# Kernel optimization log

Hardware: AMD Instinct MI355X
Metric: run time of the kernel (lower is better)

Reference implementation:

```python
import jax, jax.numpy as jnp
import numpy as np

N_BITS = 8
QMAX = float(2 ** (N_BITS - 1) - 1)  # 127 for 8-bit symmetric
EPS = 1e-8


def fake_quant(x, axes):
    """Symmetric fake quantization (quantize + dequantize) over `axes`.

    scale = amax(|x|) / qmax over the reduction axes, then
    round/clamp to the integer grid and rescale back to float.
    """
    amax = jnp.max(jnp.abs(x), axis=axes, keepdims=True)
    scale = jnp.maximum(amax, EPS) / QMAX
    q = jnp.clip(jnp.round(x / scale), -QMAX, QMAX)
    return q * scale


def setup_inputs() -> dict:
    key = jax.random.key(0)
    k1, k2, k3 = jax.random.split(key, 3)
    B, S, D_IN, D_OUT = 4, 2048, 4096, 4096
    inp = {
        "input": jax.random.normal(k1, (B, S, D_IN), dtype=jnp.float32),
        "weight": jax.random.normal(k2, (D_OUT, D_IN), dtype=jnp.float32) * (1.0 / np.sqrt(D_IN)),
        "bias": jax.random.normal(k3, (D_OUT,), dtype=jnp.float32),
    }
    return inp


def reference(input, weight, bias):
    # act quantizer: per-example scale over dims (-2, -1) i.e. (seq, hidden)
    x_q = fake_quant(input, axes=(-2, -1))
    # weight quantizer: per-tensor scale
    w_q = fake_quant(weight, axes=(0, 1))
    # F.linear: input @ weight.T + bias
    return jnp.einsum("bsi,oi->bso", x_q, w_q) + bias
```

## Files before the change

### kernel.cpp

```cpp
#include <hip/hip_runtime.h>

typedef __attribute__((ext_vector_type(4))) int i32x4;

#define AS1 __attribute__((address_space(1)))
#define AS3 __attribute__((address_space(3)))

static constexpr int  S_LEN = 2048, DIN = 4096, DOUT = 4096, NBATCH = 4;
static constexpr long XTOT = (long)NBATCH * S_LEN * DIN;
static constexpr long WTOT = (long)DOUT * DIN;
static constexpr float QMAXF = 127.0f;
static constexpr float EPSF  = 1e-8f;

__global__ __launch_bounds__(256) void amax_k(const float* __restrict__ x,
                                              const float* __restrict__ w,
                                              float* __restrict__ amax) {
  int bid = blockIdx.x;
  float m = 0.f;
  int slot;
  if (bid < 2048) {
    slot = bid >> 9;
    const float4* s = (const float4*)(x + ((long)slot << 23));
    long i = ((long)(bid & 511) << 8) + threadIdx.x;
#pragma unroll
    for (int it = 0; it < 16; ++it) {
      float4 v = s[i + (long)it * (512 * 256)];
      m = fmaxf(m, fmaxf(fmaxf(fabsf(v.x), fabsf(v.y)), fmaxf(fabsf(v.z), fabsf(v.w))));
    }
  } else {
    slot = 4;
    const float4* s = (const float4*)w;
    long i = ((long)(bid - 2048) << 8) + threadIdx.x;
#pragma unroll
    for (int it = 0; it < 16; ++it) {
      float4 v = s[i + (long)it * (1024 * 256)];
      m = fmaxf(m, fmaxf(fmaxf(fabsf(v.x), fabsf(v.y)), fmaxf(fabsf(v.z), fabsf(v.w))));
    }
  }
  for (int off = 32; off; off >>= 1) m = fmaxf(m, __shfl_xor(m, off, 64));
  __shared__ float sm[4];
  if ((threadIdx.x & 63) == 0) sm[threadIdx.x >> 6] = m;
  __syncthreads();
  if (threadIdx.x == 0) {
    m = fmaxf(fmaxf(sm[0], sm[1]), fmaxf(sm[2], sm[3]));
    atomicMax((unsigned int*)&amax[slot], __float_as_uint(m));
  }
}

__global__ __launch_bounds__(256) void quant_k(const float* __restrict__ x,
                                               const float* __restrict__ w,
                                               const float* __restrict__ amax,
                                               char* __restrict__ qx, char* __restrict__ qw) {
  long idx = ((long)blockIdx.x * blockDim.x + threadIdx.x) * 16;
  const float* src;
  char* dst;
  float scale;
  if (idx < XTOT) {
    int b = (int)(idx >> 23);
    scale = fmaxf(amax[b], EPSF) / QMAXF;
    src = x + idx;
    dst = qx + idx;
  } else {
    long j = idx - XTOT;
    scale = fmaxf(amax[4], EPSF) / QMAXF;
    src = w + j;
    dst = qw + j;
  }
  int words[4];
#pragma unroll
  for (int g = 0; g < 4; ++g) {
    float4 v = ((const float4*)src)[g];
    float r0 = fminf(fmaxf(rintf(v.x / scale), -QMAXF), QMAXF);
    float r1 = fminf(fmaxf(rintf(v.y / scale), -QMAXF), QMAXF);
    float r2 = fminf(fmaxf(rintf(v.z / scale), -QMAXF), QMAXF);
    float r3 = fminf(fmaxf(rintf(v.w / scale), -QMAXF), QMAXF);
    words[g] = ((int)r0 & 255) | (((int)r1 & 255) << 8) |
               (((int)r2 & 255) << 16) | ((int)r3 << 24);
  }
  *(i32x4*)dst = *(const i32x4*)words;
}

__device__ __forceinline__ void load_half_a(i32x4 a[4][2], const char* p, int u0, int u1) {
#pragma unroll
  for (int f = 0; f < 4; ++f) {
    a[f][0] = *(const i32x4*)(p + f * 2048 + u0);
    a[f][1] = *(const i32x4*)(p + f * 2048 + u1);
  }
}
__device__ __forceinline__ void load_half_b(i32x4 b[2][2], const char* p, int u0, int u1) {
#pragma unroll
  for (int g = 0; g < 2; ++g) {
    b[g][0] = *(const i32x4*)(p + g * 2048 + u0);
    b[g][1] = *(const i32x4*)(p + g * 2048 + u1);
  }
}
template <int QA, int QB>
__device__ __forceinline__ void do_mfma(i32x4 acc[8][4], const i32x4 a[4][2],
                                        const i32x4 b[2][2]) {
#pragma unroll
  for (int f = 0; f < 4; ++f)
#pragma unroll
    for (int g = 0; g < 2; ++g) {
      i32x4 c = acc[QA * 4 + f][QB * 2 + g];
      c = __builtin_amdgcn_mfma_i32_16x16x64_i8(a[f][0], b[g][0], c, 0, 0, 0);
      c = __builtin_amdgcn_mfma_i32_16x16x64_i8(a[f][1], b[g][1], c, 0, 0, 0);
      acc[QA * 4 + f][QB * 2 + g] = c;
    }
}
__device__ __forceinline__ void stage2(const char* g0, long K, char* ld) {
  __builtin_amdgcn_global_load_lds((const AS1 void*)g0, (AS3 void*)ld, 16, 0, 0);
  __builtin_amdgcn_global_load_lds((const AS1 void*)(g0 + 64 * K), (AS3 void*)(ld + 8192), 16, 0, 0);
}

__global__ __launch_bounds__(512, 2) void gemm_k(
    const char* __restrict__ qx, const char* __restrict__ qw,
    const float* __restrict__ amax, const float* __restrict__ bias,
    float* __restrict__ out) {
  constexpr int K = 4096, N = 4096, NT = 32;
  __shared__ __align__(16) char lds[131072];
  char* ldsA = lds;
  char* ldsB = lds + 65536;

  int cpx = (int)gridDim.x >> 3;
  int sw  = ((int)blockIdx.x & 7) * cpx + ((int)blockIdx.x >> 3);
  int tm = sw >> 4, tn = sw & 15;
  long brow = (long)tm * 256, bcol = (long)tn * 256;

  int tid = threadIdx.x;
  int l = tid & 63, wid = tid >> 6;
  int wr = wid >> 2, wc = wid & 3;

  int sl = (l >> 1) & 7;
  int u0 = (((l >> 4) ^ sl)) << 4;
  int u1 = ((((l >> 4) | 4) ^ sl)) << 4;
  int rA = (wr * 128 + (l & 15)) * 128;
  int rB = (wc * 64 + (l & 15)) * 128;

  int sr0 = tid >> 3;
  int lu16 = ((tid & 7) ^ ((sr0 >> 1) & 7)) << 4;
  const char* gA = qx + (brow + sr0) * (long)K + lu16;
  const char* gB = qw + (bcol + sr0) * (long)K + lu16;

  i32x4 acc[8][4];
#pragma unroll
  for (int i = 0; i < 8; ++i)
#pragma unroll
    for (int j = 0; j < 4; ++j) acc[i][j] = 0;
  i32x4 a[4][2], b0[2][2], b1[2][2];

  stage2(gA, K, ldsA + tid * 16);
  stage2(gB, K, ldsB + tid * 16);
  stage2(gA + 128 * (long)K, K, ldsA + 16384 + tid * 16);
  stage2(gB + 128 * (long)K, K, ldsB + 16384 + tid * 16);
  stage2(gA + 128, K, ldsA + 32768 + tid * 16);
  stage2(gB + 128, K, ldsB + 32768 + tid * 16);
  asm volatile("s_waitcnt vmcnt(4)" ::: "memory");
  __builtin_amdgcn_s_barrier();

  for (int t = 0; t < NT; ++t) {
    int d = t & 1;
    const char* cA = ldsA + d * 32768;
    const char* cB = ldsB + d * 32768;
    load_half_a(a, cA + rA, u0, u1);
    load_half_b(b0, cB + rB, u0, u1);
    if (t + 1 < NT)
      stage2(gA + 128 * (long)K + (t + 1) * 128, K,
             ldsA + ((t + 1) & 1) * 32768 + 16384 + tid * 16);
    __builtin_amdgcn_s_barrier();
    asm volatile("s_waitcnt lgkmcnt(0)" ::: "memory");
    __builtin_amdgcn_s_setprio(1);
    do_mfma<0, 0>(acc, a, b0);
    __builtin_amdgcn_s_setprio(0);
    __builtin_amdgcn_s_barrier();
    load_half_b(b1, cB + rB + 4096, u0, u1);
    if (t + 1 < NT)
      stage2(gB + 128 * (long)K + (t + 1) * 128, K,
             ldsB + ((t + 1) & 1) * 32768 + 16384 + tid * 16);
    __builtin_amdgcn_s_barrier();
    asm volatile("s_waitcnt lgkmcnt(0)" ::: "memory");
    __builtin_amdgcn_s_setprio(1);
    do_mfma<0, 1>(acc, a, b1);
    __builtin_amdgcn_s_setprio(0);
    __builtin_amdgcn_s_barrier();
    load_half_a(a, cA + rA + 8192, u0, u1);
    __builtin_amdgcn_s_barrier();
    asm volatile("s_waitcnt lgkmcnt(0)" ::: "memory");
    __builtin_amdgcn_s_setprio(1);
    do_mfma<1, 1>(acc, a, b1);
    __builtin_amdgcn_s_setprio(0);
    __builtin_amdgcn_s_barrier();
    if (t + 2 < NT) {
      stage2(gA + (t + 2) * 128, K, ldsA + d * 32768 + tid * 16);
      stage2(gB + (t + 2) * 128, K, ldsB + d * 32768 + tid * 16);
    }
    __builtin_amdgcn_s_barrier();
    __builtin_amdgcn_s_setprio(1);
    do_mfma<1, 0>(acc, a, b0);
    __builtin_amdgcn_s_setprio(0);
    if (t < NT - 2) asm volatile("s_waitcnt vmcnt(4)" ::: "memory");
    else            asm volatile("s_waitcnt vmcnt(0)" ::: "memory");
    __builtin_amdgcn_s_barrier();
  }

  float ax = amax[(int)(brow >> 11)];
  float aw = amax[4];
  float scale = (fmaxf(ax, EPSF) / QMAXF) * (fmaxf(aw, EPSF) / QMAXF);
#pragma unroll
  for (int fb = 0; fb < 4; ++fb) {
    int col = (int)bcol + wc * 64 + fb * 16 + (l & 15);
    float bv = bias[col];
#pragma unroll
    for (int fa = 0; fa < 8; ++fa) {
      long r0 = brow + wr * 128 + fa * 16 + ((l >> 4) * 4);
#pragma unroll
      for (int r = 0; r < 4; ++r)
        out[(r0 + r) * N + col] = scale * (float)acc[fa][fb][r] + bv;
    }
  }
}

extern "C" void kernel_launch(void* const* d_in, const int* in_sizes, int n_in,
                              void* d_out, int out_size, void* d_ws, size_t ws_size,
                              hipStream_t stream) {
  const float* x    = (const float*)d_in[0];
  const float* w    = (const float*)d_in[1];
  const float* bias = (const float*)d_in[2];
  float* out = (float*)d_out;

  float* amax = (float*)d_ws;
  char* qx = (char*)d_ws + 256;
  char* qw = qx + XTOT;
  if (ws_size < (size_t)(256 + XTOT + WTOT)) return;

  hipMemsetAsync(d_ws, 0, 32, stream);

  amax_k<<<3072, 256, 0, stream>>>(x, w, amax);

  long total = XTOT + WTOT;
  int qblocks = (int)(total / 16 / 256);
  quant_k<<<qblocks, 256, 0, stream>>>(x, w, amax, qx, qw);

  gemm_k<<<512, 512, 0, stream>>>(qx, qw, amax, bias, out);
}
```

Measured before the change: 429.0 us.

## Replace barrier-heavy interleaved GEMM schedule with a simple one-barrier double buffer

The int8 GEMM main loop previously split each K-tile into four MFMA phases, separated by many s_barriers. Global-to-LDS loads of the tile after next were staggered across those phases. Now each iteration loads all of its LDS fragments up front and issues the whole next K-tile into the other buffer. It then runs all four MFMA groups back-to-back and ends with a single vmcnt(0) wait and barrier. This removes most of the barrier and synchronisation overhead, but cuts the prefetch depth, so global-load latency is less hidden and register pressure from holding b0 and b1 together goes up.

```diff
diff --git a/kernel.cpp b/kernel.cpp
--- a/kernel.cpp
+++ b/kernel.cpp
@@ -148,56 +148,46 @@
   i32x4 a[4][2], b0[2][2], b1[2][2];
 
   stage2(gA, K, ldsA + tid * 16);
+  stage2(gA + 128 * (long)K, K, ldsA + 16384 + tid * 16);
   stage2(gB, K, ldsB + tid * 16);
-  stage2(gA + 128 * (long)K, K, ldsA + 16384 + tid * 16);
   stage2(gB + 128 * (long)K, K, ldsB + 16384 + tid * 16);
-  stage2(gA + 128, K, ldsA + 32768 + tid * 16);
-  stage2(gB + 128, K, ldsB + 32768 + tid * 16);
-  asm volatile("s_waitcnt vmcnt(4)" ::: "memory");
+  asm volatile("s_waitcnt vmcnt(0)" ::: "memory");
   __builtin_amdgcn_s_barrier();
 
   for (int t = 0; t < NT; ++t) {
     int d = t & 1;
     const char* cA = ldsA + d * 32768;
     const char* cB = ldsB + d * 32768;
+    char* nA = ldsA + (d ^ 1) * 32768;
+    char* nB = ldsB + (d ^ 1) * 32768;
+
     load_half_a(a, cA + rA, u0, u1);
     load_half_b(b0, cB + rB, u0, u1);
-    if (t + 1 < NT)
-      stage2(gA + 128 * (long)K + (t + 1) * 128, K,
-             ldsA + ((t + 1) & 1) * 32768 + 16384 + tid * 16);
-    __builtin_amdgcn_s_barrier();
-    asm volatile("s_waitcnt lgkmcnt(0)" ::: "memory");
+    load_half_b(b1, cB + rB + 4096, u0, u1);
+
+    if (t + 1 < NT) {
+      const char* pA = gA + (t + 1) * 128;
+      const char* pB = gB + (t + 1) * 128;
+      stage2(pA, K, nA + tid * 16);
+      stage2(pA + 128 * (long)K, K, nA + 16384 + tid * 16);
+      stage2(pB, K, nB + tid * 16);
+      stage2(pB + 128 * (long)K, K, nB + 16384 + tid * 16);
+    }
+    __builtin_amdgcn_sched_barrier(0);
+
     __builtin_amdgcn_s_setprio(1);
     do_mfma<0, 0>(acc, a, b0);
-    __builtin_amdgcn_s_setprio(0);
-    __builtin_amdgcn_s_barrier();
-    load_half_b(b1, cB + rB + 4096, u0, u1);
-    if (t + 1 < NT)
-      stage2(gB + 128 * (long)K + (t + 1) * 128, K,
-             ldsB + ((t + 1) & 1) * 32768 + 16384 + tid * 16);
-    __builtin_amdgcn_s_barrier();
-    asm volatile("s_waitcnt lgkmcnt(0)" ::: "memory");
-    __builtin_amdgcn_s_setprio(1);
     do_mfma<0, 1>(acc, a, b1);
     __builtin_amdgcn_s_setprio(0);
-    __builtin_amdgcn_s_barrier();
+
     load_half_a(a, cA + rA + 8192, u0, u1);
-    __builtin_amdgcn_s_barrier();
-    asm volatile("s_waitcnt lgkmcnt(0)" ::: "memory");
+
     __builtin_amdgcn_s_setprio(1);
     do_mfma<1, 1>(acc, a, b1);
-    __builtin_amdgcn_s_setprio(0);
-    __builtin_amdgcn_s_barrier();
-    if (t + 2 < NT) {
-      stage2(gA + (t + 2) * 128, K, ldsA + d * 32768 + tid * 16);
-      stage2(gB + (t + 2) * 128, K, ldsB + d * 32768 + tid * 16);
-    }
-    __builtin_amdgcn_s_barrier();
-    __builtin_amdgcn_s_setprio(1);
     do_mfma<1, 0>(acc, a, b0);
     __builtin_amdgcn_s_setprio(0);
-    if (t < NT - 2) asm volatile("s_waitcnt vmcnt(4)" ::: "memory");
-    else            asm volatile("s_waitcnt vmcnt(0)" ::: "memory");
+
+    asm volatile("s_waitcnt vmcnt(0)" ::: "memory");
     __builtin_amdgcn_s_barrier();
   }
 
```

Measured after the change: 424.4 us. About the same (-1.1%).
